# Performance work log

Hardware: AMD Instinct MI355X
Metric: run time of the kernel (lower is better)

## Reference

```python
import jax, jax.numpy as jnp
import numpy as np

EPS = 1e-5
NUM_CLASSES = 35
STYLE_LEN = 128


def conv3x3(x, w, b):
    # x: [B,C,H,W], w: [O,I,3,3] (OIHW), SAME padding, stride 1
    y = jax.lax.conv_general_dilated(x, w, (1, 1), 'SAME',
                                     dimension_numbers=('NCHW', 'OIHW', 'NCHW'))
    return y + b[None, :, None, None]


def instance_norm(x):
    # InstanceNorm2d(affine=False): per-sample, per-channel over H,W; biased var
    mu = jnp.mean(x, axis=(2, 3), keepdims=True)
    var = jnp.mean((x - mu) ** 2, axis=(2, 3), keepdims=True)
    return (x - mu) * jax.lax.rsqrt(var + EPS)


def setup_inputs() -> dict:
    key = jax.random.key(0)
    ks = jax.random.split(key, 20)
    B, C, H, W = 4, 256, 128, 256
    J, S = NUM_CLASSES, STYLE_LEN
    s = 0.05
    inp = {
        'x': jax.random.normal(ks[0], (B, C, H, W), jnp.float32),
        'seg_labels': jax.random.randint(ks[1], (B, H, W), 0, J),
        'style_codes': jax.random.normal(ks[2], (B, J, S), jnp.float32),
        # per-class FC: fc_w[j] is [out,in] like torch Linear
        'fc_w': jax.random.normal(ks[3], (J, S, S), jnp.float32) * s,
        'fc_b': jax.random.normal(ks[4], (J, S), jnp.float32) * s,
        'conv_gamma_w': jax.random.normal(ks[5], (C, S, 3, 3), jnp.float32) * s,
        'conv_gamma_b': jax.random.normal(ks[6], (C,), jnp.float32) * s,
        'conv_beta_w': jax.random.normal(ks[7], (C, S, 3, 3), jnp.float32) * s,
        'conv_beta_b': jax.random.normal(ks[8], (C,), jnp.float32) * s,
        # SPADE (sean=True): mlp_shared conv label_nc->128, then gamma/beta 128->C
        'mlp_w': jax.random.normal(ks[9], (128, J, 3, 3), jnp.float32) * s,
        'mlp_b': jax.random.normal(ks[10], (128,), jnp.float32) * s,
        'sp_gamma_w': jax.random.normal(ks[11], (C, 128, 3, 3), jnp.float32) * s,
        'sp_gamma_b': jax.random.normal(ks[12], (C,), jnp.float32) * s,
        'sp_beta_w': jax.random.normal(ks[13], (C, 128, 3, 3), jnp.float32) * s,
        'sp_beta_b': jax.random.normal(ks[14], (C,), jnp.float32) * s,
        'blending_gamma': jnp.zeros((1,), jnp.float32),
        'blending_beta': jnp.zeros((1,), jnp.float32),
    }
    return inp


def reference(x, seg_labels, style_codes, fc_w, fc_b,
              conv_gamma_w, conv_gamma_b, conv_beta_w, conv_beta_b,
              mlp_w, mlp_b, sp_gamma_w, sp_gamma_b, sp_beta_w, sp_beta_b,
              blending_gamma, blending_beta):
    # one-hot segmap [B,J,H,W]; same resolution as x so nearest interp is identity
    segmap = jax.nn.one_hot(seg_labels, NUM_CLASSES, axis=1, dtype=x.dtype)

    normalized = instance_norm(x)

    # per-class style FC: mu[b,j,:] = relu(fc_w[j] @ style_codes[b,j] + fc_b[j])
    mu = jax.nn.relu(jnp.einsum('bjd,jod->bjo', style_codes, fc_w) + fc_b[None])
    # gather-compute-scatter: each pixel receives the style vector of its class
    middle_avg = jnp.einsum('bjhw,bjc->bchw', segmap, mu)  # [B,128,H,W]

    gamma_avg = conv3x3(middle_avg, conv_gamma_w, conv_gamma_b)
    beta_avg = conv3x3(middle_avg, conv_beta_w, conv_beta_b)

    # SPADE branch (sean): gamma/beta from segmap
    actv = jax.nn.relu(conv3x3(segmap, mlp_w, mlp_b))
    gamma_spade = conv3x3(actv, sp_gamma_w, sp_gamma_b)
    beta_spade = conv3x3(actv, sp_beta_w, sp_beta_b)

    ga = jax.nn.sigmoid(blending_gamma)[0]
    ba = jax.nn.sigmoid(blending_beta)[0]
    gamma_final = ga * gamma_avg + (1 - ga) * gamma_spade
    beta_final = ba * beta_avg + (1 - ba) * beta_spade
    return normalized * (1 + gamma_final) + beta_final
```

## Files before the change

### kernel.cpp

```cpp
#include <hip/hip_runtime.h>
#include <stdint.h>

typedef __attribute__((ext_vector_type(8))) short short8;
typedef __attribute__((ext_vector_type(4))) float f32x4;

#define HP 130
#define WPAD 258
#define CIN 256

#define AS1 __attribute__((address_space(1)))
#define AS3 __attribute__((address_space(3)))

__device__ __forceinline__ unsigned short f2bf(float f) {
  unsigned int x = __float_as_uint(f);
  x = x + 0x7fffu + ((x >> 16) & 1u);
  return (unsigned short)(x >> 16);
}

__global__ __launch_bounds__(128) void k_mu(const float* __restrict__ sty,
    const float* __restrict__ fcw, const float* __restrict__ fcb,
    float* __restrict__ mu)
{
  int bj = blockIdx.x;
  int b = bj / 35, j = bj - 35 * b;
  int o = threadIdx.x;
  __shared__ float ss[128];
  ss[o] = sty[((size_t)b * 35 + j) * 128 + o];
  __syncthreads();
  const float4* wr = (const float4*)(fcw + ((size_t)j * 128 + o) * 128);
  const float4* sv = (const float4*)ss;
  float acc = fcb[j * 128 + o];
  #pragma unroll 8
  for (int d = 0; d < 32; ++d) {
    float4 wv = wr[d], s4 = sv[d];
    acc += wv.x * s4.x + wv.y * s4.y + wv.z * s4.z + wv.w * s4.w;
  }
  mu[((size_t)b * 35 + j) * 128 + o] = fmaxf(acc, 0.f);
}

__global__ __launch_bounds__(256) void k_prep(const float* __restrict__ mlpw,
    float* __restrict__ mlpT,
    const float* __restrict__ cgb, const float* __restrict__ cbb,
    const float* __restrict__ sgb, const float* __restrict__ sbb,
    const float* __restrict__ blg, const float* __restrict__ blb,
    float* __restrict__ bias)
{
  int t = blockIdx.x * 256 + threadIdx.x;
  if (t < 40320) {
    int o = t & 127;
    int jt = t >> 7;
    mlpT[(size_t)jt * 128 + o] = mlpw[((size_t)o * 35 + (jt / 9)) * 9 + (jt % 9)];
  }
  if (t < 256) {
    float ga = 1.f / (1.f + expf(-blg[0]));
    float ba = 1.f / (1.f + expf(-blb[0]));
    bias[t]       = ga * cgb[t] + (1.f - ga) * sgb[t];
    bias[256 + t] = ba * cbb[t] + (1.f - ba) * sbb[t];
  }
}

__global__ __launch_bounds__(256) void k_pack(
    const float* __restrict__ cgw, const float* __restrict__ cbw,
    const float* __restrict__ sgw, const float* __restrict__ sbw,
    const float* __restrict__ blg, const float* __restrict__ blb,
    unsigned short* __restrict__ Wp)
{
  int gid = blockIdx.x * 256 + threadIdx.x;
  int lane = gid & 63;
  int cc = (gid >> 6) & 7;
  int rest = gid >> 9;
  int tap = rest % 9;
  int vf = rest / 9;
  int v = vf * 16 + (lane & 15);
  int c = v >> 1, g = v & 1;
  int ci0 = cc * 32 + (lane >> 4) * 8;
  float ga = 1.f / (1.f + expf(-blg[0]));
  float ba = 1.f / (1.f + expf(-blb[0]));
  float sc = g ? ba : ga;
  const float* wavg = g ? cbw : cgw;
  const float* wsp  = g ? sbw : sgw;
  union { uint4 v4; unsigned short s[8]; } u;
  #pragma unroll
  for (int jj = 0; jj < 8; ++jj) {
    int ci = ci0 + jj;
    float val;
    if (ci < 128) val = sc * wavg[((size_t)c * 128 + ci) * 9 + tap];
    else          val = (1.f - sc) * wsp[((size_t)c * 128 + (ci - 128)) * 9 + tap];
    u.s[jj] = f2bf(val);
  }
  int vfgrp = vf >> 2, mfi = vf & 3;
  uint4* dst = (uint4*)Wp + ((size_t)(((vfgrp * 8 + cc) * 9 + tap) * 4 + mfi)) * 64 + lane;
  *dst = u.v4;
}

__global__ __launch_bounds__(256) void k_stats(const float* __restrict__ x,
                                               float* __restrict__ stats)
{
  int bc = blockIdx.x;
  const float* p = x + (size_t)bc * 32768;
  int t = threadIdx.x;
  float s = 0.f, s2 = 0.f;
  #pragma unroll 4
  for (int i = 0; i < 32; ++i) {
    float4 v = *(const float4*)(p + (size_t)i * 1024 + t * 4);
    s  += v.x + v.y + v.z + v.w;
    s2 += v.x * v.x + v.y * v.y + v.z * v.z + v.w * v.w;
  }
  #pragma unroll
  for (int off2 = 32; off2 > 0; off2 >>= 1) {
    s  += __shfl_down(s, off2);
    s2 += __shfl_down(s2, off2);
  }
  __shared__ float red[8];
  int lane = t & 63, wv = t >> 6;
  if (lane == 0) { red[wv] = s; red[4 + wv] = s2; }
  __syncthreads();
  if (t == 0) {
    float S  = red[0] + red[1] + red[2] + red[3];
    float S2 = red[4] + red[5] + red[6] + red[7];
    float mean = S * (1.f / 32768.f);
    float var  = S2 * (1.f / 32768.f) - mean * mean;
    stats[bc] = mean;
    stats[1024 + bc] = rsqrtf(var + 1e-5f);
  }
}

__global__ __launch_bounds__(256) void k_build(const int* __restrict__ seg,
    const float* __restrict__ mu, const float* __restrict__ mlpT,
    const float* __restrict__ mlpb, unsigned short* __restrict__ U)
{
  int blk = blockIdx.x;
  int b = blk >> 12, rem = blk & 4095;
  int h = rem >> 5, w0 = (rem & 31) << 3;
  int t = threadIdx.x;
  int p = t >> 5, q = t & 31;
  int w = w0 + p;
  unsigned short* up = U + (((size_t)(b * HP + h + 1)) * WPAD + (w + 1)) * CIN;
  union { uint4 v4; unsigned short s[8]; } u;
  if (q < 16) {
    int lab = seg[((size_t)b * 128 + h) * 256 + w];
    const float4* mrow = (const float4*)(mu + ((size_t)(b * 35 + lab)) * 128 + q * 8);
    float4 v0 = mrow[0], v1 = mrow[1];
    u.s[0] = f2bf(v0.x); u.s[1] = f2bf(v0.y); u.s[2] = f2bf(v0.z); u.s[3] = f2bf(v0.w);
    u.s[4] = f2bf(v1.x); u.s[5] = f2bf(v1.y); u.s[6] = f2bf(v1.z); u.s[7] = f2bf(v1.w);
    *(uint4*)(up + q * 8) = u.v4;
  } else {
    int o0 = (q - 16) * 8;
    float a[8];
    #pragma unroll
    for (int j = 0; j < 8; ++j) a[j] = mlpb[o0 + j];
    #pragma unroll
    for (int kh = 0; kh < 3; ++kh) {
      int hh = h + kh - 1;
      if ((unsigned)hh < 128u) {
        #pragma unroll
        for (int kw = 0; kw < 3; ++kw) {
          int ww = w + kw - 1;
          if ((unsigned)ww < 256u) {
            int lab2 = seg[((size_t)b * 128 + hh) * 256 + ww];
            const float4* wr = (const float4*)(mlpT + ((size_t)lab2 * 9 + kh * 3 + kw) * 128 + o0);
            float4 v0 = wr[0], v1 = wr[1];
            a[0] += v0.x; a[1] += v0.y; a[2] += v0.z; a[3] += v0.w;
            a[4] += v1.x; a[5] += v1.y; a[6] += v1.z; a[7] += v1.w;
          }
        }
      }
    }
    #pragma unroll
    for (int j = 0; j < 8; ++j) u.s[j] = f2bf(fmaxf(a[j], 0.f));
    *(uint4*)(up + 128 + o0) = u.v4;
  }
}


#define WAITV_(vm, lg) asm volatile("s_waitcnt vmcnt(" #vm ") lgkmcnt(" #lg ")" ::: "memory")
#define WAITV(vm, lg) do { WAITV_(vm, lg); __builtin_amdgcn_sched_barrier(0); } while (0)

#define MM(CS) do {                                                            \
    __builtin_amdgcn_s_setprio(1);                                             \
    _Pragma("unroll")                                                          \
    for (int mf_ = 0; mf_ < 4; ++mf_)                                          \
      _Pragma("unroll")                                                        \
      for (int nf_ = 0; nf_ < 4; ++nf_)                                        \
        acc[mf_][nf_] = __builtin_amdgcn_mfma_f32_16x16x32_bf16(               \
            afr##CS[mf_], bfr##CS[nf_], acc[mf_][nf_], 0, 0, 0);               \
    __builtin_amdgcn_s_setprio(0);                                             \
  } while (0)

#define LOADA(NS) do {                                                         \
    aptr += 4096;                                                              \
    afr##NS[0] = *(const short8*)(aptr);                                       \
    afr##NS[1] = *(const short8*)(aptr + 1024);                                \
    afr##NS[2] = *(const short8*)(aptr + 2048);                                \
    afr##NS[3] = *(const short8*)(aptr + 3072);                                \
  } while (0)

#define LOADB(NS, T1) do {                                                     \
    bfr##NS[0] = *(const short8*)(lbuf + off[T1]);                             \
    bfr##NS[1] = *(const short8*)(lbuf + off[T1] + 1024);                      \
    bfr##NS[2] = *(const short8*)(lbuf + off[T1] + 2048);                      \
    bfr##NS[3] = *(const short8*)(lbuf + off[T1] + 3072);                      \
  } while (0)

#define STG(SI) do {                                                           \
    __builtin_amdgcn_global_load_lds((const AS1 unsigned int*)gsrc[SI],        \
        (AS3 unsigned int*)((SI) < 6 ? (stbw + (SI) * 4096) : (stb + 24576)),  \
        16, 0, 0);                                                             \
    gsrc[SI] += 64;                                                            \
  } while (0)

__global__ __launch_bounds__(256, 3) void k_conv(
    const float* __restrict__ x, const uint4* __restrict__ U,
    const char* __restrict__ Wp, const float* __restrict__ bias,
    const float* __restrict__ stats, float* __restrict__ out)
{
  int bid = blockIdx.x;
  int xcd = bid & 7, i0 = bid >> 3;
  int pt = xcd * 128 + (i0 >> 2);
  int mt = i0 & 3;
  int b = pt >> 8, rem = pt & 255;
  int h0 = rem >> 1, w0 = (rem & 1) << 7;
  int tid = threadIdx.x;
  int lane = tid & 63, wid = tid >> 6;
  int lo = lane & 15, hi = lane >> 4;
  int wm = wid >> 1, wn = wid & 1;

  __shared__ uint4 Ubuf[2][1600];

  const char* gsrc[7];
  #pragma unroll
  for (int i = 0; i < 7; ++i) {
    int row = (i < 6) ? (wid + 4 * i) : 24;
    int slot = row * 64 + lane;
    int P = slot >> 2, sp = slot & 3;
    int sl = sp ^ ((P >> 1) & 3);
    int r = P / 130, pix = P - r * 130;
    gsrc[i] = (const char*)U +
        (size_t)(((b * HP + h0 + r) * WPAD + (w0 + pix)) * CIN + sl * 8) * 2;
  }

  f32x4 acc[4][4];
  #pragma unroll
  for (int i = 0; i < 4; ++i)
    #pragma unroll
    for (int j = 0; j < 4; ++j) acc[i][j] = (f32x4){0.f, 0.f, 0.f, 0.f};

  int vfgrp = mt * 2 + wm;
  const char* aptr = Wp + (size_t)vfgrp * 294912 + lane * 16;

  int pb = wn * 64 + lo;
  int off[9];
  #pragma unroll
  for (int t = 0; t < 9; ++t) {
    int Pb = (t / 3) * 130 + (t % 3) + pb;
    off[t] = Pb * 64 + ((hi ^ ((Pb >> 1) & 3)) << 4);
  }

  const char* lbuf = (const char*)&Ubuf[0][0];
  char* stb = (char*)&Ubuf[1][0];

  {
    char* stb0 = (char*)&Ubuf[0][0];
    char* stbw0 = stb0 + wid * 1024;
    #pragma unroll
    for (int i = 0; i < 7; ++i) {
      __builtin_amdgcn_global_load_lds((const AS1 unsigned int*)gsrc[i],
          (AS3 unsigned int*)(i < 6 ? (stbw0 + i * 4096) : (stb0 + 24576)), 16, 0, 0);
      gsrc[i] += 64;
    }
  }
  short8 afr0[4], afr1[4], bfr0[4], bfr1[4];
  afr0[0] = *(const short8*)(aptr);
  afr0[1] = *(const short8*)(aptr + 1024);
  afr0[2] = *(const short8*)(aptr + 2048);
  afr0[3] = *(const short8*)(aptr + 3072);
  WAITV(4, 0);
  __builtin_amdgcn_s_barrier();

  #pragma unroll 1
  for (int cc = 0; cc < 7; ++cc) {
    char* stbw = stb + wid * 1024;
    LOADB(0, 0);
    LOADA(1); STG(0); LOADB(1, 1); WAITV(5, 4); MM(0);
    LOADA(0); STG(1); LOADB(0, 2); WAITV(6, 4); MM(1);
    LOADA(1); STG(2); LOADB(1, 3); WAITV(6, 4); MM(0);
    LOADA(0); STG(3); LOADB(0, 4); WAITV(6, 4); MM(1);
    LOADA(1); STG(4); LOADB(1, 5); WAITV(6, 4); MM(0);
    LOADA(0); STG(5); LOADB(0, 6); WAITV(6, 4); MM(1);
    LOADA(1); STG(6); LOADB(1, 7); WAITV(6, 4); MM(0);
    LOADA(0);         LOADB(0, 8); WAITV(5, 4); MM(1);
    LOADA(1);                      WAITV(4, 0); MM(0);
    __builtin_amdgcn_s_barrier();
    { const char* tmp = lbuf; lbuf = (const char*)stb; stb = (char*)tmp; }
    { short8 t0 = afr1[0]; afr0[0] = t0; t0 = afr1[1]; afr0[1] = t0;
      t0 = afr1[2]; afr0[2] = t0; t0 = afr1[3]; afr0[3] = t0; }
  }
  {
    LOADB(0, 0);
    LOADA(1); LOADB(1, 1); WAITV(4, 4); MM(0);
    LOADA(0); LOADB(0, 2); WAITV(4, 4); MM(1);
    LOADA(1); LOADB(1, 3); WAITV(4, 4); MM(0);
    LOADA(0); LOADB(0, 4); WAITV(4, 4); MM(1);
    LOADA(1); LOADB(1, 5); WAITV(4, 4); MM(0);
    LOADA(0); LOADB(0, 6); WAITV(4, 4); MM(1);
    LOADA(1); LOADB(1, 7); WAITV(4, 4); MM(0);
    LOADA(0); LOADB(0, 8); WAITV(4, 4); MM(1);
                           WAITV(0, 0); MM(0);
  }

  #pragma unroll
  for (int mf = 0; mf < 4; ++mf) {
    int vbase = mt * 128 + wm * 64 + mf * 16 + hi * 4;
    #pragma unroll
    for (int p = 0; p < 2; ++p) {
      int c = (vbase >> 1) + p;
      float bg = bias[c], bb = bias[256 + c];
      float mean = stats[b * 256 + c], rs = stats[1024 + b * 256 + c];
      const float* xrow = x + ((size_t)(b * 256 + c) * 128 + h0) * 256 + w0 + wn * 64;
      float* orow = out + ((size_t)(b * 256 + c) * 128 + h0) * 256 + w0 + wn * 64;
      #pragma unroll
      for (int nf = 0; nf < 4; ++nf) {
        int pix = nf * 16 + lo;
        float g  = acc[mf][nf][2 * p]     + bg;
        float bt = acc[mf][nf][2 * p + 1] + bb;
        float xv = xrow[pix];
        orow[pix] = (xv - mean) * rs * (1.f + g) + bt;
      }
    }
  }
}

extern "C" void kernel_launch(void* const* d_in, const int* in_sizes, int n_in,
                              void* d_out, int out_size, void* d_ws, size_t ws_size,
                              hipStream_t stream)
{
  const float* x    = (const float*)d_in[0];
  const int*   seg  = (const int*)d_in[1];
  const float* sty  = (const float*)d_in[2];
  const float* fcw  = (const float*)d_in[3];
  const float* fcb  = (const float*)d_in[4];
  const float* cgw  = (const float*)d_in[5];
  const float* cgb  = (const float*)d_in[6];
  const float* cbw  = (const float*)d_in[7];
  const float* cbb  = (const float*)d_in[8];
  const float* mlpw = (const float*)d_in[9];
  const float* mlpb = (const float*)d_in[10];
  const float* sgw  = (const float*)d_in[11];
  const float* sgb  = (const float*)d_in[12];
  const float* sbw  = (const float*)d_in[13];
  const float* sbb  = (const float*)d_in[14];
  const float* blg  = (const float*)d_in[15];
  const float* blb  = (const float*)d_in[16];
  float* out = (float*)d_out;

  char* ws = (char*)d_ws;
  const size_t U_BYTES = (size_t)4 * HP * WPAD * CIN * 2;
  size_t off = 0;
  unsigned short* U = (unsigned short*)(ws + off); off += U_BYTES + 262144;
  char* Wp   = ws + off;           off += (size_t)512 * 256 * 9 * 2;
  float* mu  = (float*)(ws + off); off += (size_t)4 * 35 * 128 * 4;
  float* mlpT= (float*)(ws + off); off += (size_t)35 * 9 * 128 * 4;
  float* bias= (float*)(ws + off); off += 2048;
  float* stats=(float*)(ws + off); off += 8192;
  if (ws_size < off) return;

  hipMemsetAsync(U, 0, U_BYTES, stream);
  k_mu   <<<dim3(140),     dim3(128), 0, stream>>>(sty, fcw, fcb, mu);
  k_prep <<<dim3(158),     dim3(256), 0, stream>>>(mlpw, mlpT, cgb, cbb, sgb, sbb, blg, blb, bias);
  k_pack <<<dim3(576),     dim3(256), 0, stream>>>(cgw, cbw, sgw, sbw, blg, blb, (unsigned short*)Wp);
  k_stats<<<dim3(1024),    dim3(256), 0, stream>>>(x, stats);
  k_build<<<dim3(16384),   dim3(256), 0, stream>>>(seg, mu, mlpT, mlpb, U);
  k_conv <<<dim3(4096),    dim3(256), 0, stream>>>(x, (const uint4*)U, Wp, bias, stats, out);
}
```

Before: 384.9 us.

## Enlarge conv block tile to 256 channels by 128 pixels per workgroup

Each k_conv workgroup now computes 256 output rows (gamma/beta interleaved) over 128 pixels instead of 128 over 128. Every wave owns a 64x128 tile with twice as many accumulators, and B fragments are loaded in two halves. This halves the grid, so the staged input tile in LDS is reused across twice as many output channels and total LDS/global traffic for U drops by half. In exchange, register pressure roughly doubles, occupancy falls from 3 to 2 blocks per CU, and the software pipeline gains extra LDS waits.

```diff
diff --git a/kernel.cpp b/kernel.cpp
--- a/kernel.cpp
+++ b/kernel.cpp
@@ -175,15 +175,16 @@
 
 #define WAITV_(vm, lg) asm volatile("s_waitcnt vmcnt(" #vm ") lgkmcnt(" #lg ")" ::: "memory")
 #define WAITV(vm, lg) do { WAITV_(vm, lg); __builtin_amdgcn_sched_barrier(0); } while (0)
-
-#define MM(CS) do {                                                            \
+#define WAITL(lg) do { asm volatile("s_waitcnt lgkmcnt(" #lg ")" ::: "memory"); __builtin_amdgcn_sched_barrier(0); } while (0)
+
+#define MM(AS, BS, H) do {                                                     \
     __builtin_amdgcn_s_setprio(1);                                             \
     _Pragma("unroll")                                                          \
     for (int mf_ = 0; mf_ < 4; ++mf_)                                          \
       _Pragma("unroll")                                                        \
       for (int nf_ = 0; nf_ < 4; ++nf_)                                        \
-        acc[mf_][nf_] = __builtin_amdgcn_mfma_f32_16x16x32_bf16(               \
-            afr##CS[mf_], bfr##CS[nf_], acc[mf_][nf_], 0, 0, 0);               \
+        acc[mf_][(H) * 4 + nf_] = __builtin_amdgcn_mfma_f32_16x16x32_bf16(     \
+            afr##AS[mf_], bfr##BS[nf_], acc[mf_][(H) * 4 + nf_], 0, 0, 0);     \
     __builtin_amdgcn_s_setprio(0);                                             \
   } while (0)
 
@@ -195,11 +196,11 @@
     afr##NS[3] = *(const short8*)(aptr + 3072);                                \
   } while (0)
 
-#define LOADB(NS, T1) do {                                                     \
-    bfr##NS[0] = *(const short8*)(lbuf + off[T1]);                             \
-    bfr##NS[1] = *(const short8*)(lbuf + off[T1] + 1024);                      \
-    bfr##NS[2] = *(const short8*)(lbuf + off[T1] + 2048);                      \
-    bfr##NS[3] = *(const short8*)(lbuf + off[T1] + 3072);                      \
+#define LOADB(NS, T, H) do {                                                   \
+    bfr##NS[0] = *(const short8*)(lbuf + off[T] + (H) * 4096);                 \
+    bfr##NS[1] = *(const short8*)(lbuf + off[T] + (H) * 4096 + 1024);          \
+    bfr##NS[2] = *(const short8*)(lbuf + off[T] + (H) * 4096 + 2048);          \
+    bfr##NS[3] = *(const short8*)(lbuf + off[T] + (H) * 4096 + 3072);          \
   } while (0)
 
 #define STG(SI) do {                                                           \
@@ -209,21 +210,20 @@
     gsrc[SI] += 64;                                                            \
   } while (0)
 
-__global__ __launch_bounds__(256, 3) void k_conv(
+__global__ __launch_bounds__(256, 2) void k_conv(
     const float* __restrict__ x, const uint4* __restrict__ U,
     const char* __restrict__ Wp, const float* __restrict__ bias,
     const float* __restrict__ stats, float* __restrict__ out)
 {
   int bid = blockIdx.x;
   int xcd = bid & 7, i0 = bid >> 3;
-  int pt = xcd * 128 + (i0 >> 2);
-  int mt = i0 & 3;
+  int pt = xcd * 128 + (i0 >> 1);
+  int mt = i0 & 1;
   int b = pt >> 8, rem = pt & 255;
   int h0 = rem >> 1, w0 = (rem & 1) << 7;
   int tid = threadIdx.x;
   int lane = tid & 63, wid = tid >> 6;
   int lo = lane & 15, hi = lane >> 4;
-  int wm = wid >> 1, wn = wid & 1;
 
   __shared__ uint4 Ubuf[2][1600];
 
@@ -239,20 +239,19 @@
         (size_t)(((b * HP + h0 + r) * WPAD + (w0 + pix)) * CIN + sl * 8) * 2;
   }
 
-  f32x4 acc[4][4];
+  f32x4 acc[4][8];
   #pragma unroll
   for (int i = 0; i < 4; ++i)
     #pragma unroll
-    for (int j = 0; j < 4; ++j) acc[i][j] = (f32x4){0.f, 0.f, 0.f, 0.f};
-
-  int vfgrp = mt * 2 + wm;
+    for (int j = 0; j < 8; ++j) acc[i][j] = (f32x4){0.f, 0.f, 0.f, 0.f};
+
+  int vfgrp = mt * 4 + wid;
   const char* aptr = Wp + (size_t)vfgrp * 294912 + lane * 16;
 
-  int pb = wn * 64 + lo;
   int off[9];
   #pragma unroll
   for (int t = 0; t < 9; ++t) {
-    int Pb = (t / 3) * 130 + (t % 3) + pb;
+    int Pb = (t / 3) * 130 + (t % 3) + lo;
     off[t] = Pb * 64 + ((hi ^ ((Pb >> 1) & 3)) << 4);
   }
 
@@ -280,46 +279,64 @@
   #pragma unroll 1
   for (int cc = 0; cc < 7; ++cc) {
     char* stbw = stb + wid * 1024;
-    LOADB(0, 0);
-    LOADA(1); STG(0); LOADB(1, 1); WAITV(5, 4); MM(0);
-    LOADA(0); STG(1); LOADB(0, 2); WAITV(6, 4); MM(1);
-    LOADA(1); STG(2); LOADB(1, 3); WAITV(6, 4); MM(0);
-    LOADA(0); STG(3); LOADB(0, 4); WAITV(6, 4); MM(1);
-    LOADA(1); STG(4); LOADB(1, 5); WAITV(6, 4); MM(0);
-    LOADA(0); STG(5); LOADB(0, 6); WAITV(6, 4); MM(1);
-    LOADA(1); STG(6); LOADB(1, 7); WAITV(6, 4); MM(0);
-    LOADA(0);         LOADB(0, 8); WAITV(5, 4); MM(1);
-    LOADA(1);                      WAITV(4, 0); MM(0);
+    LOADB(0, 0, 0);
+    LOADA(1); STG(0); LOADB(1, 0, 1); WAITV(5, 4); MM(0, 0, 0);
+              LOADB(0, 1, 0);        WAITL(4);     MM(0, 1, 1);
+    LOADA(0); STG(1); LOADB(1, 1, 1); WAITV(5, 4); MM(1, 0, 0);
+              LOADB(0, 2, 0);        WAITL(4);     MM(1, 1, 1);
+    LOADA(1); STG(2); LOADB(1, 2, 1); WAITV(5, 4); MM(0, 0, 0);
+              LOADB(0, 3, 0);        WAITL(4);     MM(0, 1, 1);
+    LOADA(0); STG(3); LOADB(1, 3, 1); WAITV(5, 4); MM(1, 0, 0);
+              LOADB(0, 4, 0);        WAITL(4);     MM(1, 1, 1);
+    LOADA(1); STG(4); LOADB(1, 4, 1); WAITV(5, 4); MM(0, 0, 0);
+              LOADB(0, 5, 0);        WAITL(4);     MM(0, 1, 1);
+    LOADA(0); STG(5); LOADB(1, 5, 1); WAITV(5, 4); MM(1, 0, 0);
+              LOADB(0, 6, 0);        WAITL(4);     MM(1, 1, 1);
+    LOADA(1); STG(6); LOADB(1, 6, 1); WAITV(5, 4); MM(0, 0, 0);
+              LOADB(0, 7, 0);        WAITL(4);     MM(0, 1, 1);
+    LOADA(0);         LOADB(1, 7, 1); WAITV(5, 4); MM(1, 0, 0);
+              LOADB(0, 8, 0);        WAITL(4);     MM(1, 1, 1);
+    LOADA(1);         LOADB(1, 8, 1); WAITV(4, 4); MM(0, 0, 0);
+                                     WAITV(4, 0);  MM(0, 1, 1);
     __builtin_amdgcn_s_barrier();
     { const char* tmp = lbuf; lbuf = (const char*)stb; stb = (char*)tmp; }
     { short8 t0 = afr1[0]; afr0[0] = t0; t0 = afr1[1]; afr0[1] = t0;
       t0 = afr1[2]; afr0[2] = t0; t0 = afr1[3]; afr0[3] = t0; }
   }
   {
-    LOADB(0, 0);
-    LOADA(1); LOADB(1, 1); WAITV(4, 4); MM(0);
-    LOADA(0); LOADB(0, 2); WAITV(4, 4); MM(1);
-    LOADA(1); LOADB(1, 3); WAITV(4, 4); MM(0);
-    LOADA(0); LOADB(0, 4); WAITV(4, 4); MM(1);
-    LOADA(1); LOADB(1, 5); WAITV(4, 4); MM(0);
-    LOADA(0); LOADB(0, 6); WAITV(4, 4); MM(1);
-    LOADA(1); LOADB(1, 7); WAITV(4, 4); MM(0);
-    LOADA(0); LOADB(0, 8); WAITV(4, 4); MM(1);
-                           WAITV(0, 0); MM(0);
+    LOADB(0, 0, 0);
+    LOADA(1); LOADB(1, 0, 1); WAITV(4, 4); MM(0, 0, 0);
+              LOADB(0, 1, 0); WAITL(4);    MM(0, 1, 1);
+    LOADA(0); LOADB(1, 1, 1); WAITV(4, 4); MM(1, 0, 0);
+              LOADB(0, 2, 0); WAITL(4);    MM(1, 1, 1);
+    LOADA(1); LOADB(1, 2, 1); WAITV(4, 4); MM(0, 0, 0);
+              LOADB(0, 3, 0); WAITL(4);    MM(0, 1, 1);
+    LOADA(0); LOADB(1, 3, 1); WAITV(4, 4); MM(1, 0, 0);
+              LOADB(0, 4, 0); WAITL(4);    MM(1, 1, 1);
+    LOADA(1); LOADB(1, 4, 1); WAITV(4, 4); MM(0, 0, 0);
+              LOADB(0, 5, 0); WAITL(4);    MM(0, 1, 1);
+    LOADA(0); LOADB(1, 5, 1); WAITV(4, 4); MM(1, 0, 0);
+              LOADB(0, 6, 0); WAITL(4);    MM(1, 1, 1);
+    LOADA(1); LOADB(1, 6, 1); WAITV(4, 4); MM(0, 0, 0);
+              LOADB(0, 7, 0); WAITL(4);    MM(0, 1, 1);
+    LOADA(0); LOADB(1, 7, 1); WAITV(4, 4); MM(1, 0, 0);
+              LOADB(0, 8, 0); WAITL(4);    MM(1, 1, 1);
+              LOADB(1, 8, 1); WAITV(0, 4); MM(0, 0, 0);
+                              WAITL(0);    MM(0, 1, 1);
   }
 
   #pragma unroll
   for (int mf = 0; mf < 4; ++mf) {
-    int vbase = mt * 128 + wm * 64 + mf * 16 + hi * 4;
+    int vbase = mt * 256 + wid * 64 + mf * 16 + hi * 4;
     #pragma unroll
     for (int p = 0; p < 2; ++p) {
       int c = (vbase >> 1) + p;
       float bg = bias[c], bb = bias[256 + c];
       float mean = stats[b * 256 + c], rs = stats[1024 + b * 256 + c];
-      const float* xrow = x + ((size_t)(b * 256 + c) * 128 + h0) * 256 + w0 + wn * 64;
-      float* orow = out + ((size_t)(b * 256 + c) * 128 + h0) * 256 + w0 + wn * 64;
+      const float* xrow = x + ((size_t)(b * 256 + c) * 128 + h0) * 256 + w0;
+      float* orow = out + ((size_t)(b * 256 + c) * 128 + h0) * 256 + w0;
       #pragma unroll
-      for (int nf = 0; nf < 4; ++nf) {
+      for (int nf = 0; nf < 8; ++nf) {
         int pix = nf * 16 + lo;
         float g  = acc[mf][nf][2 * p]     + bg;
         float bt = acc[mf][nf][2 * p + 1] + bb;
@@ -370,5 +387,5 @@
   k_pack <<<dim3(576),     dim3(256), 0, stream>>>(cgw, cbw, sgw, sbw, blg, blb, (unsigned short*)Wp);
   k_stats<<<dim3(1024),    dim3(256), 0, stream>>>(x, stats);
   k_build<<<dim3(16384),   dim3(256), 0, stream>>>(seg, mu, mlpT, mlpb, U);
-  k_conv <<<dim3(4096),    dim3(256), 0, stream>>>(x, (const uint4*)U, Wp, bias, stats, out);
-}
+  k_conv <<<dim3(2048),    dim3(256), 0, stream>>>(x, (const uint4*)U, Wp, bias, stats, out);
+}
```

Result: faster. 344.0 us (-10.6%).
